# Performance work log

Measured on AMD Instinct MI355X. Metric: run time of the kernel, lower is better.

Reference implementation:

```python
import jax, jax.numpy as jnp
import numpy as np

HIDDEN = 512
EXP = 2048  # hidden * expansion_factor(4)

def _glorot(key, shape):
    fan_in = shape[0]
    return jax.random.normal(key, shape, dtype=jnp.float32) / np.sqrt(fan_in)

def setup_inputs() -> dict:
    key = jax.random.key(0)
    ks = jax.random.split(key, 6)
    B, S = 4, 4096
    return {
        "x": jax.random.normal(ks[0], (B, S, HIDDEN), dtype=jnp.float32),
        "W_in1": _glorot(ks[1], (HIDDEN, EXP)),
        "b_in1": jnp.zeros((EXP,), jnp.float32),
        "W_in2": _glorot(ks[2], (HIDDEN, EXP)),
        "b_in2": jnp.zeros((EXP,), jnp.float32),
        "W_z": _glorot(ks[3], (EXP, EXP)),
        "b_z": jnp.zeros((EXP,), jnp.float32),
        "W_h": _glorot(ks[4], (EXP, EXP)),
        "b_h": jnp.zeros((EXP,), jnp.float32),
        "W_out": _glorot(ks[5], (EXP, HIDDEN)),
        "b_out": jnp.zeros((HIDDEN,), jnp.float32),
    }

def _min_gru(x_in, W_z, b_z, W_h, b_h):
    # minGRU: h_t = (1 - z_t) * h_{t-1} + z_t * h_tilde_t, h_0 = 0
    z = jax.nn.sigmoid(jnp.einsum("bse,ef->bsf", x_in, W_z) + b_z)
    h_tilde = jnp.einsum("bse,ef->bsf", x_in, W_h) + b_h
    a = 1.0 - z          # decay coeff
    b = z * h_tilde      # input term
    def combine(c1, c2):
        a1, b1 = c1
        a2, b2 = c2
        return (a1 * a2, b1 * a2 + b2)
    _, h = jax.lax.associative_scan(combine, (a, b), axis=1)
    return h

def reference(x, W_in1, b_in1, W_in2, b_in2, W_z, b_z, W_h, b_h, W_out, b_out):
    x_in = jax.nn.silu(jnp.einsum("bsd,de->bse", x, W_in1) + b_in1)
    x_skip = jax.nn.silu(jnp.einsum("bsd,de->bse", x, W_in2) + b_in2)
    h = _min_gru(x_in, W_z, b_z, W_h, b_h)
    return jnp.einsum("bse,ed->bsd", x_skip + h, W_out) + b_out
```

## Files before the change

### kernel.cpp

```cpp
#include <hip/hip_runtime.h>
#include <hip/hip_bf16.h>


typedef __bf16 bf16x8 __attribute__((ext_vector_type(8)));
typedef __bf16 bf16x4 __attribute__((ext_vector_type(4)));
typedef float  f32x4  __attribute__((ext_vector_type(4)));

#define DEVINL __device__ __forceinline__

DEVINL void async_ld16(const __bf16* g, __bf16* l) {
    __builtin_amdgcn_global_load_lds(
        (const __attribute__((address_space(1))) void*)g,
        (__attribute__((address_space(3))) void*)l, 16, 0, 0);
}

DEVINL float fsigmoid(float v) { return 1.0f / (1.0f + __expf(-v)); }

template <int MODE>
__global__ __launch_bounds__(256)
void gemm_bt64(const __bf16* __restrict__ A, const __bf16* __restrict__ Bt,
               const float* __restrict__ bias, const float* __restrict__ bias2,
               void* __restrict__ out, void* __restrict__ out2, int N, int K,
               int bps, int seg_stride, int row_off)
{
    struct KL64 { __bf16 A[128 * 64]; __bf16 B[128 * 64]; };
    __shared__ union SMB64 {
        KL64 kl[2];
        __bf16 ct[64 * 136];
    } sm;
    const int tid = threadIdx.x;
    const int bx = blockIdx.x;
    const int seg = bx / bps;
    const int within = bx - seg * bps;
    const int gm0 = row_off + seg * seg_stride + within * 128;
    const int om0 = bx * 128;
    const int n0 = blockIdx.y * 128;

    int rS[4], kS[4];
#pragma unroll
    for (int j = 0; j < 4; ++j) {
        const int s = tid + 256 * j;
        rS[j] = s >> 3;
        kS[j] = (s & 7) ^ (rS[j] & 7);
    }
    const __bf16* Agp[4];
    const __bf16* Bgp[4];
#pragma unroll
    for (int j = 0; j < 4; ++j) {
        Agp[j] = A  + (size_t)(gm0 + rS[j]) * K + kS[j] * 8;
        Bgp[j] = Bt + (size_t)(n0 + rS[j]) * K + kS[j] * 8;
    }

    const int lane = tid & 63;
    const int wave = tid >> 6;
    const int wrow = (wave >> 1) * 64;
    const int wcol = (wave & 1) * 64;
    const int quad = lane >> 4;
    const int r = lane & 15;

    f32x4 acc[4][4] = {};

    const int T = K >> 6;

    auto stage = [&](int t, int b) {
        const int kt = t << 6;
#pragma unroll
        for (int j = 0; j < 4; ++j)
            async_ld16(Agp[j] + kt, sm.kl[b].A + (tid + 256 * j) * 8);
#pragma unroll
        for (int j = 0; j < 4; ++j)
            async_ld16(Bgp[j] + kt, sm.kl[b].B + (tid + 256 * j) * 8);
    };

    stage(0, 0);

    const int swz0 = ((0 * 4 + quad) ^ (r & 7)) * 8;
    const int swz1 = ((1 * 4 + quad) ^ (r & 7)) * 8;

    for (int t = 0; t < T; ++t) {
        const int cur = t & 1;
        if (t + 1 < T) {
            stage(t + 1, cur ^ 1);
            asm volatile("s_waitcnt vmcnt(8)\n\ts_barrier" ::: "memory");
        } else {
            asm volatile("s_waitcnt vmcnt(0)\n\ts_barrier" ::: "memory");
        }

        const __bf16* apb = sm.kl[cur].A + (wrow + r) * 64;
        const __bf16* bpb = sm.kl[cur].B + (wcol + r) * 64;

#pragma unroll
        for (int ks = 0; ks < 2; ++ks) {
            const int swz = ks ? swz1 : swz0;
            bf16x8 af[4], bf_[4];
#pragma unroll
            for (int m = 0; m < 4; ++m)
                af[m] = *(const bf16x8*)(apb + m * 1024 + swz);
#pragma unroll
            for (int n = 0; n < 4; ++n)
                bf_[n] = *(const bf16x8*)(bpb + n * 1024 + swz);

            __builtin_amdgcn_s_setprio(1);
#pragma unroll
            for (int m = 0; m < 4; ++m)
#pragma unroll
                for (int n = 0; n < 4; ++n)
                    acc[m][n] = __builtin_amdgcn_mfma_f32_16x16x32_bf16(
                        af[m], bf_[n], acc[m][n], 0, 0, 0);
            __builtin_amdgcn_s_setprio(0);
        }

        asm volatile("s_waitcnt lgkmcnt(0)\n\ts_barrier" ::: "memory");
    }

    {
        const bool lo = n0 < 2048;
        __bf16* dst = lo ? (__bf16*)out : (__bf16*)out2;
        const int cb = lo ? n0 : n0 - 2048;
        const size_t stride = 2048;
        float bvj[4];
#pragma unroll
        for (int j = 0; j < 4; ++j) {
            const int gc = n0 + wcol + j * 16 + r;
            bvj[j] = lo ? bias[gc] : bias2[gc - 2048];
        }
#pragma unroll
        for (int p = 0; p < 2; ++p) {
#pragma unroll
            for (int ii = 0; ii < 2; ++ii) {
                const int i = 2 * p + ii;
#pragma unroll
                for (int j = 0; j < 4; ++j)
#pragma unroll
                    for (int k = 0; k < 4; ++k) {
                        const float v = acc[i][j][k] + bvj[j];
                        const __bf16 o = (__bf16)(v * fsigmoid(v));
                        sm.ct[((wave >> 1) * 32 + ii * 16 + quad * 4 + k) * 136 +
                              (wcol + j * 16 + r)] = o;
                    }
            }
            __syncthreads();
#pragma unroll
            for (int q = 0; q < 4; ++q) {
                const int chunk = q * 256 + tid;
                const int trow = chunk >> 4;
                const int tc = (chunk & 15) * 8;
                const bf16x8 vv = *(const bf16x8*)(sm.ct + trow * 136 + tc);
                const int grow = om0 + (trow >> 5) * 64 + p * 32 + (trow & 31);
                *(bf16x8*)(dst + (size_t)grow * stride + cb + tc) = vv;
            }
            __syncthreads();
        }
    }
}

template <int MODE>
__global__ __launch_bounds__(512, 2)
void gemm3k(const __bf16* __restrict__ A, const __bf16* __restrict__ Bt,
            const float* __restrict__ bias, const float* __restrict__ bias2,
            void* __restrict__ out, void* __restrict__ out2, int N, int K,
            int bps, int seg_stride, int row_off)
{
    struct KL { __bf16 A[256 * 64]; __bf16 B[256 * 64]; };
    __shared__ union SM3K {
        KL kl[2];
        __bf16 ct[64 * 264];
    } sm;
    const int tid = threadIdx.x;
    const int bx = blockIdx.x;
    const int seg = bx / bps;
    const int within = bx - seg * bps;
    const int gm0 = row_off + seg * seg_stride + within * 256;
    const int om0 = bx * 256;
    const int n0 = blockIdx.y * 256;

    int rA[4], kA[4];
#pragma unroll
    for (int j = 0; j < 4; ++j) {
        const int s = tid + 512 * j;
        rA[j] = s >> 3;
        kA[j] = (s & 7) ^ (rA[j] & 7);
    }
    const __bf16* Agp[4];
    const __bf16* Bgp[4];
#pragma unroll
    for (int j = 0; j < 4; ++j) {
        Agp[j] = A  + (size_t)(gm0 + rA[j]) * K + kA[j] * 8;
        Bgp[j] = Bt + (size_t)(n0 + rA[j]) * K + kA[j] * 8;
    }

    const int lane = tid & 63;
    const int wave = tid >> 6;
    const int wm = wave >> 2;
    const int wn = wave & 3;
    const int quad = lane >> 4;
    const int r = lane & 15;

    f32x4 acc[8][4] = {};

    const int T = K >> 6;

    auto stage = [&](int t, int b) {
        const int kt = t << 6;
#pragma unroll
        for (int j = 0; j < 4; ++j)
            async_ld16(Agp[j] + kt, sm.kl[b].A + (tid + 512 * j) * 8);
#pragma unroll
        for (int j = 0; j < 4; ++j)
            async_ld16(Bgp[j] + kt, sm.kl[b].B + (tid + 512 * j) * 8);
    };

    stage(0, 0);

    const int swz0 = ((0 * 4 + quad) ^ (r & 7)) * 8;
    const int swz1 = ((1 * 4 + quad) ^ (r & 7)) * 8;

    for (int t = 0; t < T; ++t) {
        const int cur = t & 1;
        if (t + 1 < T) {
            stage(t + 1, cur ^ 1);
            asm volatile("s_waitcnt vmcnt(8)\n\ts_barrier" ::: "memory");
        } else {
            asm volatile("s_waitcnt vmcnt(0)\n\ts_barrier" ::: "memory");
        }

        const __bf16* apb = sm.kl[cur].A + (wm * 128 + r) * 64;
        const __bf16* bpb = sm.kl[cur].B + (wn * 64 + r) * 64;

#pragma unroll
        for (int ks = 0; ks < 2; ++ks) {
            const int swz = ks ? swz1 : swz0;
            bf16x8 af[8], bf_[4];
#pragma unroll
            for (int m = 0; m < 8; ++m)
                af[m] = *(const bf16x8*)(apb + m * 1024 + swz);
#pragma unroll
            for (int n = 0; n < 4; ++n)
                bf_[n] = *(const bf16x8*)(bpb + n * 1024 + swz);

            __builtin_amdgcn_s_setprio(1);
#pragma unroll
            for (int m = 0; m < 8; ++m)
#pragma unroll
                for (int n = 0; n < 4; ++n)
                    acc[m][n] = __builtin_amdgcn_mfma_f32_16x16x32_bf16(
                        af[m], bf_[n], acc[m][n], 0, 0, 0);
            __builtin_amdgcn_s_setprio(0);
        }

        asm volatile("s_waitcnt lgkmcnt(0)\n\ts_barrier" ::: "memory");
    }

    __syncthreads();

    const bool lo = n0 < 2048;
    __bf16* dst = (__bf16*)out;
    const int cb = n0;
    const size_t stride = (size_t)N;
    float bvj[4];
#pragma unroll
    for (int nf = 0; nf < 4; ++nf) {
        const int gc = n0 + wn * 64 + nf * 16 + r;
        bvj[nf] = lo ? bias[gc] : bias2[gc - 2048];
    }

#pragma unroll
    for (int p = 0; p < 4; ++p) {
        if (wm == (p >> 1)) {
            const int mb = (p & 1) * 4;
#pragma unroll
            for (int mm = 0; mm < 4; ++mm)
#pragma unroll
                for (int nf = 0; nf < 4; ++nf)
#pragma unroll
                    for (int k = 0; k < 4; ++k) {
                        const float v = acc[mb + mm][nf][k] + bvj[nf];
                        sm.ct[(mm * 16 + quad * 4 + k) * 264 +
                              (wn * 64 + nf * 16 + r)] = (__bf16)v;
                    }
        }
        __syncthreads();
#pragma unroll
        for (int q = 0; q < 4; ++q) {
            const int chunk = q * 512 + tid;
            const int trow = chunk >> 5;
            const int tc = (chunk & 31) * 8;
            const bf16x8 vv = *(const bf16x8*)(sm.ct + trow * 264 + tc);
            *(bf16x8*)(dst + (size_t)(om0 + p * 64 + trow) * stride + cb + tc) = vv;
        }
        __syncthreads();
    }
}

struct KLoopSM { __bf16 A[2][128 * 32]; __bf16 B[2][128 * 32]; };

template <int MODE>
__global__ __launch_bounds__(256)
void gemm_bt(const __bf16* __restrict__ A, const __bf16* __restrict__ Bt,
             const float* __restrict__ bias, const float* __restrict__ bias2,
             void* __restrict__ out, void* __restrict__ out2, int N, int K,
             int bps, int seg_stride, int row_off)
{
    __shared__ union SM {
        KLoopSM kl;
        __bf16 ct[64 * 136];
        float  ctf[32 * 132];
    } sm;
    const int tid = threadIdx.x;
    const int bx = blockIdx.x;
    const int by = blockIdx.y;
    const int seg = bx / bps;
    const int within = bx - seg * bps;
    const int gm0 = row_off + seg * seg_stride + within * 128;
    const int om0 = bx * 128;
    const int n0 = by * 128;

    const int c0 = tid, c1 = tid + 256;
    const int r0 = c0 >> 2, k0 = (c0 & 3) ^ ((c0 >> 3) & 3);
    const int r1 = c1 >> 2, k1 = (c1 & 3) ^ ((c1 >> 3) & 3);
    const __bf16* Ag0 = A  + (size_t)(gm0 + r0) * K + k0 * 8;
    const __bf16* Ag1 = A  + (size_t)(gm0 + r1) * K + k1 * 8;
    const __bf16* Bg0 = Bt + (size_t)(n0 + r0) * K + k0 * 8;
    const __bf16* Bg1 = Bt + (size_t)(n0 + r1) * K + k1 * 8;

    const int lane = tid & 63;
    const int wave = tid >> 6;
    const int wrow = (wave >> 1) * 64;
    const int wcol = (wave & 1) * 64;
    const int quad = lane >> 4;
    const int r = lane & 15;
    const int swz = (quad ^ ((r >> 1) & 3)) * 8;

    f32x4 acc[4][4] = {};

    const int T = K >> 5;
    async_ld16(Ag0, sm.kl.A[0] + c0 * 8);
    async_ld16(Ag1, sm.kl.A[0] + c1 * 8);
    async_ld16(Bg0, sm.kl.B[0] + c0 * 8);
    async_ld16(Bg1, sm.kl.B[0] + c1 * 8);

    for (int t = 0; t < T; ++t) {
        const int cur = t & 1;
        if (t + 1 < T) {
            const int kt = (t + 1) << 5;
            async_ld16(Ag0 + kt, sm.kl.A[cur ^ 1] + c0 * 8);
            async_ld16(Ag1 + kt, sm.kl.A[cur ^ 1] + c1 * 8);
            async_ld16(Bg0 + kt, sm.kl.B[cur ^ 1] + c0 * 8);
            async_ld16(Bg1 + kt, sm.kl.B[cur ^ 1] + c1 * 8);
            asm volatile("s_waitcnt vmcnt(4)\n\ts_barrier" ::: "memory");
        } else {
            asm volatile("s_waitcnt vmcnt(0)\n\ts_barrier" ::: "memory");
        }

        const __bf16* ap = sm.kl.A[cur] + (wrow + r) * 32 + swz;
        const __bf16* bp = sm.kl.B[cur] + (wcol + r) * 32 + swz;
        bf16x8 af[4], bf_[4];
#pragma unroll
        for (int i = 0; i < 4; ++i) af[i] = *(const bf16x8*)(ap + i * 512);
#pragma unroll
        for (int i = 0; i < 4; ++i) bf_[i] = *(const bf16x8*)(bp + i * 512);
#pragma unroll
        for (int i = 0; i < 4; ++i)
#pragma unroll
            for (int j = 0; j < 4; ++j)
                acc[i][j] = __builtin_amdgcn_mfma_f32_16x16x32_bf16(
                    af[i], bf_[j], acc[i][j], 0, 0, 0);

        asm volatile("s_waitcnt lgkmcnt(0)\n\ts_barrier" ::: "memory");
    }

    if (MODE == 3) {
        float bvj[4];
#pragma unroll
        for (int j = 0; j < 4; ++j)
            bvj[j] = bias[n0 + wcol + j * 16 + r];
#pragma unroll
        for (int p = 0; p < 4; ++p) {
#pragma unroll
            for (int j = 0; j < 4; ++j)
#pragma unroll
                for (int k = 0; k < 4; ++k)
                    sm.ctf[((wave >> 1) * 16 + quad * 4 + k) * 132 +
                           (wcol + j * 16 + r)] = acc[p][j][k] + bvj[j];
            __syncthreads();
#pragma unroll
            for (int q = 0; q < 4; ++q) {
                const int chunk = q * 256 + tid;
                const int trow = chunk >> 5;
                const int tc4 = (chunk & 31) * 4;
                const f32x4 vv = *(const f32x4*)(sm.ctf + trow * 132 + tc4);
                const int grow = om0 + (trow >> 4) * 64 + p * 16 + (trow & 15);
                *(f32x4*)((float*)out + (size_t)grow * N + n0 + tc4) = vv;
            }
            __syncthreads();
        }
    } else {
        const bool lo = n0 < 2048;
        __bf16* dst;
        int cb;
        size_t stride;
        if (MODE == 0) {
            dst = lo ? (__bf16*)out : (__bf16*)out2;
            cb = lo ? n0 : n0 - 2048;
            stride = 2048;
        } else {
            dst = (__bf16*)out;
            cb = n0;
            stride = (size_t)N;
        }
        float bvj[4];
#pragma unroll
        for (int j = 0; j < 4; ++j) {
            const int gc = n0 + wcol + j * 16 + r;
            bvj[j] = lo ? bias[gc] : bias2[gc - 2048];
        }
#pragma unroll
        for (int p = 0; p < 2; ++p) {
#pragma unroll
            for (int ii = 0; ii < 2; ++ii) {
                const int i = 2 * p + ii;
#pragma unroll
                for (int j = 0; j < 4; ++j)
#pragma unroll
                    for (int k = 0; k < 4; ++k) {
                        const float v = acc[i][j][k] + bvj[j];
                        const __bf16 o = (MODE == 0) ? (__bf16)(v * fsigmoid(v))
                                                     : (__bf16)v;
                        sm.ct[((wave >> 1) * 32 + ii * 16 + quad * 4 + k) * 136 +
                              (wcol + j * 16 + r)] = o;
                    }
            }
            __syncthreads();
#pragma unroll
            for (int q = 0; q < 4; ++q) {
                const int chunk = q * 256 + tid;
                const int trow = chunk >> 4;
                const int tc = (chunk & 15) * 8;
                const bf16x8 vv = *(const bf16x8*)(sm.ct + trow * 136 + tc);
                const int grow = om0 + (trow >> 5) * 64 + p * 32 + (trow & 31);
                *(bf16x8*)(dst + (size_t)grow * stride + cb + tc) = vv;
            }
            __syncthreads();
        }
    }
}

#define SSEG 32
#define SCOLS 32
__global__ __launch_bounds__(1024)
void scan_kernel(const __bf16* __restrict__ raw, __bf16* __restrict__ xskip,
                 float* __restrict__ carry, int CS, int S, int t0, int first)
{
    __shared__ float Als[SSEG][SCOLS];
    __shared__ float Bls[SSEG][SCOLS];
    const int lane = threadIdx.x & (SCOLS - 1);
    const int w = threadIdx.x >> 5;
    const int nb8 = gridDim.x >> 3;
    const int lin = (blockIdx.x & 7) * nb8 + (blockIdx.x >> 3);
    const int gpb = 2048 / SCOLS;
    const int batch = lin / gpb;
    const int col = (lin - batch * gpb) * SCOLS + lane;
    const int L = CS / SSEG;
    const int tbeg = w * L;

    const size_t rbase = ((size_t)batch * CS + tbeg) * 4096 + col;

    float av[32], bv[32];
    float A = 1.0f, Bv = 0.0f;
    {
        size_t idx = rbase;
#pragma unroll
        for (int t = 0; t < 32; ++t, idx += 4096) {
            const float z = fsigmoid((float)raw[idx]);
            const float b = z * (float)raw[idx + 2048];
            const float a = 1.0f - z;
            av[t] = a;
            bv[t] = b;
            Bv = a * Bv + b;
            A *= a;
        }
    }
    Als[w][lane] = A;
    Bls[w][lane] = Bv;
    __syncthreads();

    const int ch = batch * 2048 + col;
    float h = first ? 0.0f : carry[ch];
    for (int s = 0; s < w; ++s)
        h = Als[s][lane] * h + Bls[s][lane];
    if (w == SSEG - 1)
        carry[ch] = A * h + Bv;

    {
        size_t gidx = ((size_t)batch * S + t0 + tbeg) * 2048 + col;
#pragma unroll
        for (int t = 0; t < 32; ++t, gidx += 2048) {
            h = av[t] * h + bv[t];
            xskip[gidx] = (__bf16)((float)xskip[gidx] + h);
        }
    }
}

__global__ __launch_bounds__(256)
void conv_f32_bf16(const float* __restrict__ x, __bf16* __restrict__ y, int n4)
{
    const int i = blockIdx.x * 256 + threadIdx.x;
    if (i >= n4) return;
    const float4 v = ((const float4*)x)[i];
    bf16x4 o;
    o[0] = (__bf16)v.x; o[1] = (__bf16)v.y; o[2] = (__bf16)v.z; o[3] = (__bf16)v.w;
    ((bf16x4*)y)[i] = o;
}

__global__ __launch_bounds__(256)
void transpose_bf16(const float* __restrict__ W, __bf16* __restrict__ Wt, int K, int N)
{
    __shared__ float tile[32][33];
    const int tx = threadIdx.x & 31;
    const int ty = threadIdx.x >> 5;
    const int nb = blockIdx.x * 32;
    const int kb = blockIdx.y * 32;
#pragma unroll
    for (int i = 0; i < 32; i += 8)
        tile[ty + i][tx] = W[(size_t)(kb + ty + i) * N + nb + tx];
    __syncthreads();
#pragma unroll
    for (int i = 0; i < 32; i += 8)
        Wt[(size_t)(nb + ty + i) * K + kb + tx] = (__bf16)tile[tx][ty + i];
}

extern "C" void kernel_launch(void* const* d_in, const int* in_sizes, int n_in,
                              void* d_out, int out_size, void* d_ws, size_t ws_size,
                              hipStream_t stream)
{
    const float* x     = (const float*)d_in[0];
    const float* W_in1 = (const float*)d_in[1];
    const float* b_in1 = (const float*)d_in[2];
    const float* W_in2 = (const float*)d_in[3];
    const float* b_in2 = (const float*)d_in[4];
    const float* W_z   = (const float*)d_in[5];
    const float* b_z   = (const float*)d_in[6];
    const float* W_h   = (const float*)d_in[7];
    const float* b_h   = (const float*)d_in[8];
    const float* W_out = (const float*)d_in[9];
    const float* b_out = (const float*)d_in[10];

    const int B = 4, S = 4096, H = 512, E = 2048;
    const int M = B * S;
    const int CS = 1024;
    const int NC = S / CS;
    const int MC = B * CS;

    const size_t MiB = 1024 * 1024;
    const size_t NEEDED = 183 * MiB;
    if (ws_size < NEEDED) return;

    char* ws = (char*)d_ws;
    __bf16* xb    = (__bf16*)(ws + 0);
    __bf16* rawzh = (__bf16*)(ws + 0);
    float*  carry = (float*) (ws + 32 * MiB);
    __bf16* xin   = (__bf16*)(ws + 33 * MiB);
    __bf16* xskip = (__bf16*)(ws + 97 * MiB);
    __bf16* Wt12  = (__bf16*)(ws + 161 * MiB);
    __bf16* Wtzh  = (__bf16*)(ws + 165 * MiB);
    __bf16* Wto   = (__bf16*)(ws + 181 * MiB);

    conv_f32_bf16<<<(M * H / 4 + 255) / 256, 256, 0, stream>>>(x, xb, M * H / 4);
    transpose_bf16<<<dim3(E / 32, H / 32), 256, 0, stream>>>(W_in1, Wt12, H, E);
    transpose_bf16<<<dim3(E / 32, H / 32), 256, 0, stream>>>(W_in2, Wt12 + (size_t)E * H, H, E);
    transpose_bf16<<<dim3(E / 32, E / 32), 256, 0, stream>>>(W_z, Wtzh, E, E);
    transpose_bf16<<<dim3(E / 32, E / 32), 256, 0, stream>>>(W_h, Wtzh + (size_t)E * E, E, E);
    transpose_bf16<<<dim3(H / 32, E / 32), 256, 0, stream>>>(W_out, Wto, E, H);

    gemm_bt64<0><<<dim3(M / 128, 2 * E / 128), 256, 0, stream>>>(
        xb, Wt12, b_in1, b_in2, xin, xskip, 2 * E, H, M / 128, 0, 0);

    for (int c = 0; c < NC; ++c) {
        const int row_off = c * CS;
        gemm3k<4><<<dim3(MC / 256, 2 * E / 256), 512, 0, stream>>>(
            xin, Wtzh, b_z, b_h, rawzh, nullptr, 2 * E, E, CS / 256, S, row_off);
        scan_kernel<<<(B * E) / SCOLS, 1024, 0, stream>>>(
            rawzh, xskip, carry, CS, S, row_off, c == 0);
    }

    gemm_bt<3><<<dim3(M / 128, H / 128), 256, 0, stream>>>(
        xskip, Wto, b_out, nullptr, (float*)d_out, nullptr, H, E, M / 128, 0, 0);
}
```

Baseline: 613.5 us.

## Retile input GEMM, use BK64 kernel for output GEMM, fuse prep kernels

The input projection GEMM now runs as a 512-thread kernel with 128x256 tiles and BK=32 in place of 128x128 tiles with BK=64. The output GEMM moves from a BK=32 loop to the BK=64 double-buffered kernel with swizzled 8-chunk layout. The x conversion and five weight transposes are merged into one prep_kernel launch to cut launch overhead. Together these aim to raise MFMA efficiency and reduce per-launch cost, at the price of different occupancy and LDS pressure.

New measurement: 574.7 us. 6.3% less time.

```diff
diff --git a/kernel.cpp b/kernel.cpp
--- a/kernel.cpp
+++ b/kernel.cpp
@@ -17,16 +17,16 @@
 DEVINL float fsigmoid(float v) { return 1.0f / (1.0f + __expf(-v)); }
 
 template <int MODE>
-__global__ __launch_bounds__(256)
-void gemm_bt64(const __bf16* __restrict__ A, const __bf16* __restrict__ Bt,
-               const float* __restrict__ bias, const float* __restrict__ bias2,
-               void* __restrict__ out, void* __restrict__ out2, int N, int K,
-               int bps, int seg_stride, int row_off)
+__global__ __launch_bounds__(512, 4)
+void gemm4(const __bf16* __restrict__ A, const __bf16* __restrict__ Bt,
+           const float* __restrict__ bias, const float* __restrict__ bias2,
+           void* __restrict__ out, void* __restrict__ out2, int N, int K,
+           int bps, int seg_stride, int row_off)
 {
-    struct KL64 { __bf16 A[128 * 64]; __bf16 B[128 * 64]; };
-    __shared__ union SMB64 {
-        KL64 kl[2];
-        __bf16 ct[64 * 136];
+    struct KL { __bf16 A[128 * 32]; __bf16 B[256 * 32]; };
+    __shared__ union SM4 {
+        KL kl[2];
+        __bf16 ct[64 * 264];
     } sm;
     const int tid = threadIdx.x;
     const int bx = blockIdx.x;
@@ -34,123 +34,112 @@
     const int within = bx - seg * bps;
     const int gm0 = row_off + seg * seg_stride + within * 128;
     const int om0 = bx * 128;
-    const int n0 = blockIdx.y * 128;
-
-    int rS[4], kS[4];
-#pragma unroll
-    for (int j = 0; j < 4; ++j) {
-        const int s = tid + 256 * j;
-        rS[j] = s >> 3;
-        kS[j] = (s & 7) ^ (rS[j] & 7);
-    }
-    const __bf16* Agp[4];
-    const __bf16* Bgp[4];
-#pragma unroll
-    for (int j = 0; j < 4; ++j) {
-        Agp[j] = A  + (size_t)(gm0 + rS[j]) * K + kS[j] * 8;
-        Bgp[j] = Bt + (size_t)(n0 + rS[j]) * K + kS[j] * 8;
-    }
+    const int n0 = blockIdx.y * 256;
+
+    const int rA = tid >> 2,         kA = (tid & 3) ^ ((tid >> 3) & 3);
+    const int c0 = tid, c1 = tid + 512;
+    const int rB0 = c0 >> 2,         kB0 = (c0 & 3) ^ ((c0 >> 3) & 3);
+    const int rB1 = c1 >> 2,         kB1 = (c1 & 3) ^ ((c1 >> 3) & 3);
+    const __bf16* Ag  = A  + (size_t)(gm0 + rA)  * K + kA  * 8;
+    const __bf16* Bg0 = Bt + (size_t)(n0 + rB0) * K + kB0 * 8;
+    const __bf16* Bg1 = Bt + (size_t)(n0 + rB1) * K + kB1 * 8;
 
     const int lane = tid & 63;
     const int wave = tid >> 6;
-    const int wrow = (wave >> 1) * 64;
-    const int wcol = (wave & 1) * 64;
+    const int wm = wave >> 2;
+    const int wn = wave & 3;
     const int quad = lane >> 4;
     const int r = lane & 15;
+    const int swz = (quad ^ ((r >> 1) & 3)) * 8;
 
     f32x4 acc[4][4] = {};
 
-    const int T = K >> 6;
+    const int T = K >> 5;
 
     auto stage = [&](int t, int b) {
-        const int kt = t << 6;
-#pragma unroll
-        for (int j = 0; j < 4; ++j)
-            async_ld16(Agp[j] + kt, sm.kl[b].A + (tid + 256 * j) * 8);
-#pragma unroll
-        for (int j = 0; j < 4; ++j)
-            async_ld16(Bgp[j] + kt, sm.kl[b].B + (tid + 256 * j) * 8);
+        const int kt = t << 5;
+        async_ld16(Ag  + kt, sm.kl[b].A + tid * 8);
+        async_ld16(Bg0 + kt, sm.kl[b].B + c0 * 8);
+        async_ld16(Bg1 + kt, sm.kl[b].B + c1 * 8);
     };
 
     stage(0, 0);
-
-    const int swz0 = ((0 * 4 + quad) ^ (r & 7)) * 8;
-    const int swz1 = ((1 * 4 + quad) ^ (r & 7)) * 8;
 
     for (int t = 0; t < T; ++t) {
         const int cur = t & 1;
         if (t + 1 < T) {
             stage(t + 1, cur ^ 1);
-            asm volatile("s_waitcnt vmcnt(8)\n\ts_barrier" ::: "memory");
+            asm volatile("s_waitcnt vmcnt(3)\n\ts_barrier" ::: "memory");
         } else {
             asm volatile("s_waitcnt vmcnt(0)\n\ts_barrier" ::: "memory");
         }
 
-        const __bf16* apb = sm.kl[cur].A + (wrow + r) * 64;
-        const __bf16* bpb = sm.kl[cur].B + (wcol + r) * 64;
-
-#pragma unroll
-        for (int ks = 0; ks < 2; ++ks) {
-            const int swz = ks ? swz1 : swz0;
-            bf16x8 af[4], bf_[4];
-#pragma unroll
-            for (int m = 0; m < 4; ++m)
-                af[m] = *(const bf16x8*)(apb + m * 1024 + swz);
+        const __bf16* ap = sm.kl[cur].A + (wm * 64 + r) * 32 + swz;
+        const __bf16* bp = sm.kl[cur].B + (wn * 64 + r) * 32 + swz;
+        bf16x8 af[4], bf_[4];
+#pragma unroll
+        for (int m = 0; m < 4; ++m) af[m] = *(const bf16x8*)(ap + m * 512);
+#pragma unroll
+        for (int n = 0; n < 4; ++n) bf_[n] = *(const bf16x8*)(bp + n * 512);
+
+        __builtin_amdgcn_s_setprio(1);
+#pragma unroll
+        for (int m = 0; m < 4; ++m)
 #pragma unroll
             for (int n = 0; n < 4; ++n)
-                bf_[n] = *(const bf16x8*)(bpb + n * 1024 + swz);
-
-            __builtin_amdgcn_s_setprio(1);
-#pragma unroll
-            for (int m = 0; m < 4; ++m)
-#pragma unroll
-                for (int n = 0; n < 4; ++n)
-                    acc[m][n] = __builtin_amdgcn_mfma_f32_16x16x32_bf16(
-                        af[m], bf_[n], acc[m][n], 0, 0, 0);
-            __builtin_amdgcn_s_setprio(0);
-        }
+                acc[m][n] = __builtin_amdgcn_mfma_f32_16x16x32_bf16(
+                    af[m], bf_[n], acc[m][n], 0, 0, 0);
+        __builtin_amdgcn_s_setprio(0);
 
         asm volatile("s_waitcnt lgkmcnt(0)\n\ts_barrier" ::: "memory");
     }
 
-    {
-        const bool lo = n0 < 2048;
-        __bf16* dst = lo ? (__bf16*)out : (__bf16*)out2;
-        const int cb = lo ? n0 : n0 - 2048;
-        const size_t stride = 2048;
-        float bvj[4];
-#pragma unroll
-        for (int j = 0; j < 4; ++j) {
-            const int gc = n0 + wcol + j * 16 + r;
-            bvj[j] = lo ? bias[gc] : bias2[gc - 2048];
-        }
-#pragma unroll
-        for (int p = 0; p < 2; ++p) {
-#pragma unroll
-            for (int ii = 0; ii < 2; ++ii) {
-                const int i = 2 * p + ii;
-#pragma unroll
-                for (int j = 0; j < 4; ++j)
+    const bool lo = n0 < 2048;
+    __bf16* dst;
+    int cb;
+    size_t stride;
+    if (MODE == 0) {
+        dst = lo ? (__bf16*)out : (__bf16*)out2;
+        cb = lo ? n0 : n0 - 2048;
+        stride = 2048;
+    } else {
+        dst = (__bf16*)out;
+        cb = n0;
+        stride = (size_t)N;
+    }
+    float bvj[4];
+#pragma unroll
+    for (int nf = 0; nf < 4; ++nf) {
+        const int gc = n0 + wn * 64 + nf * 16 + r;
+        bvj[nf] = lo ? bias[gc] : bias2[gc - 2048];
+    }
+
+#pragma unroll
+    for (int p = 0; p < 2; ++p) {
+        if (wm == p) {
+#pragma unroll
+            for (int mm = 0; mm < 4; ++mm)
+#pragma unroll
+                for (int nf = 0; nf < 4; ++nf)
 #pragma unroll
                     for (int k = 0; k < 4; ++k) {
-                        const float v = acc[i][j][k] + bvj[j];
-                        const __bf16 o = (__bf16)(v * fsigmoid(v));
-                        sm.ct[((wave >> 1) * 32 + ii * 16 + quad * 4 + k) * 136 +
-                              (wcol + j * 16 + r)] = o;
+                        const float v = acc[mm][nf][k] + bvj[nf];
+                        const __bf16 o = (MODE == 0) ? (__bf16)(v * fsigmoid(v))
+                                                     : (__bf16)v;
+                        sm.ct[(mm * 16 + quad * 4 + k) * 264 +
+                              (wn * 64 + nf * 16 + r)] = o;
                     }
-            }
-            __syncthreads();
-#pragma unroll
-            for (int q = 0; q < 4; ++q) {
-                const int chunk = q * 256 + tid;
-                const int trow = chunk >> 4;
-                const int tc = (chunk & 15) * 8;
-                const bf16x8 vv = *(const bf16x8*)(sm.ct + trow * 136 + tc);
-                const int grow = om0 + (trow >> 5) * 64 + p * 32 + (trow & 31);
-                *(bf16x8*)(dst + (size_t)grow * stride + cb + tc) = vv;
-            }
-            __syncthreads();
-        }
+        }
+        __syncthreads();
+#pragma unroll
+        for (int q = 0; q < 4; ++q) {
+            const int chunk = q * 512 + tid;
+            const int trow = chunk >> 5;
+            const int tc = (chunk & 31) * 8;
+            const bf16x8 vv = *(const bf16x8*)(sm.ct + trow * 264 + tc);
+            *(bf16x8*)(dst + (size_t)(om0 + p * 64 + trow) * stride + cb + tc) = vv;
+        }
+        __syncthreads();
     }
 }
 
@@ -292,36 +281,40 @@
     }
 }
 
-struct KLoopSM { __bf16 A[2][128 * 32]; __bf16 B[2][128 * 32]; };
-
 template <int MODE>
 __global__ __launch_bounds__(256)
-void gemm_bt(const __bf16* __restrict__ A, const __bf16* __restrict__ Bt,
-             const float* __restrict__ bias, const float* __restrict__ bias2,
-             void* __restrict__ out, void* __restrict__ out2, int N, int K,
-             int bps, int seg_stride, int row_off)
+void gemm_bt64(const __bf16* __restrict__ A, const __bf16* __restrict__ Bt,
+               const float* __restrict__ bias, const float* __restrict__ bias2,
+               void* __restrict__ out, void* __restrict__ out2, int N, int K,
+               int bps, int seg_stride, int row_off)
 {
-    __shared__ union SM {
-        KLoopSM kl;
-        __bf16 ct[64 * 136];
+    struct KL64 { __bf16 A[128 * 64]; __bf16 B[128 * 64]; };
+    __shared__ union SMB64 {
+        KL64 kl[2];
         float  ctf[32 * 132];
     } sm;
     const int tid = threadIdx.x;
     const int bx = blockIdx.x;
-    const int by = blockIdx.y;
     const int seg = bx / bps;
     const int within = bx - seg * bps;
     const int gm0 = row_off + seg * seg_stride + within * 128;
     const int om0 = bx * 128;
-    const int n0 = by * 128;
-
-    const int c0 = tid, c1 = tid + 256;
-    const int r0 = c0 >> 2, k0 = (c0 & 3) ^ ((c0 >> 3) & 3);
-    const int r1 = c1 >> 2, k1 = (c1 & 3) ^ ((c1 >> 3) & 3);
-    const __bf16* Ag0 = A  + (size_t)(gm0 + r0) * K + k0 * 8;
-    const __bf16* Ag1 = A  + (size_t)(gm0 + r1) * K + k1 * 8;
-    const __bf16* Bg0 = Bt + (size_t)(n0 + r0) * K + k0 * 8;
-    const __bf16* Bg1 = Bt + (size_t)(n0 + r1) * K + k1 * 8;
+    const int n0 = blockIdx.y * 128;
+
+    int rS[4], kS[4];
+#pragma unroll
+    for (int j = 0; j < 4; ++j) {
+        const int s = tid + 256 * j;
+        rS[j] = s >> 3;
+        kS[j] = (s & 7) ^ (rS[j] & 7);
+    }
+    const __bf16* Agp[4];
+    const __bf16* Bgp[4];
+#pragma unroll
+    for (int j = 0; j < 4; ++j) {
+        Agp[j] = A  + (size_t)(gm0 + rS[j]) * K + kS[j] * 8;
+        Bgp[j] = Bt + (size_t)(n0 + rS[j]) * K + kS[j] * 8;
+    }
 
     const int lane = tid & 63;
     const int wave = tid >> 6;
@@ -329,47 +322,63 @@
     const int wcol = (wave & 1) * 64;
     const int quad = lane >> 4;
     const int r = lane & 15;
-    const int swz = (quad ^ ((r >> 1) & 3)) * 8;
 
     f32x4 acc[4][4] = {};
 
-    const int T = K >> 5;
-    async_ld16(Ag0, sm.kl.A[0] + c0 * 8);
-    async_ld16(Ag1, sm.kl.A[0] + c1 * 8);
-    async_ld16(Bg0, sm.kl.B[0] + c0 * 8);
-    async_ld16(Bg1, sm.kl.B[0] + c1 * 8);
+    const int T = K >> 6;
+
+    auto stage = [&](int t, int b) {
+        const int kt = t << 6;
+#pragma unroll
+        for (int j = 0; j < 4; ++j)
+            async_ld16(Agp[j] + kt, sm.kl[b].A + (tid + 256 * j) * 8);
+#pragma unroll
+        for (int j = 0; j < 4; ++j)
+            async_ld16(Bgp[j] + kt, sm.kl[b].B + (tid + 256 * j) * 8);
+    };
+
+    stage(0, 0);
+
+    const int swz0 = ((0 * 4 + quad) ^ (r & 7)) * 8;
+    const int swz1 = ((1 * 4 + quad) ^ (r & 7)) * 8;
 
     for (int t = 0; t < T; ++t) {
         const int cur = t & 1;
         if (t + 1 < T) {
-            const int kt = (t + 1) << 5;
-            async_ld16(Ag0 + kt, sm.kl.A[cur ^ 1] + c0 * 8);
-            async_ld16(Ag1 + kt, sm.kl.A[cur ^ 1] + c1 * 8);
-            async_ld16(Bg0 + kt, sm.kl.B[cur ^ 1] + c0 * 8);
-            async_ld16(Bg1 + kt, sm.kl.B[cur ^ 1] + c1 * 8);
-            asm volatile("s_waitcnt vmcnt(4)\n\ts_barrier" ::: "memory");
+            stage(t + 1, cur ^ 1);
+            asm volatile("s_waitcnt vmcnt(8)\n\ts_barrier" ::: "memory");
         } else {
             asm volatile("s_waitcnt vmcnt(0)\n\ts_barrier" ::: "memory");
         }
 
-        const __bf16* ap = sm.kl.A[cur] + (wrow + r) * 32 + swz;
-        const __bf16* bp = sm.kl.B[cur] + (wcol + r) * 32 + swz;
-        bf16x8 af[4], bf_[4];
-#pragma unroll
-        for (int i = 0; i < 4; ++i) af[i] = *(const bf16x8*)(ap + i * 512);
-#pragma unroll
-        for (int i = 0; i < 4; ++i) bf_[i] = *(const bf16x8*)(bp + i * 512);
-#pragma unroll
-        for (int i = 0; i < 4; ++i)
-#pragma unroll
-            for (int j = 0; j < 4; ++j)
-                acc[i][j] = __builtin_amdgcn_mfma_f32_16x16x32_bf16(
-                    af[i], bf_[j], acc[i][j], 0, 0, 0);
+        const __bf16* apb = sm.kl[cur].A + (wrow + r) * 64;
+        const __bf16* bpb = sm.kl[cur].B + (wcol + r) * 64;
+
+#pragma unroll
+        for (int ks = 0; ks < 2; ++ks) {
+            const int swz = ks ? swz1 : swz0;
+            bf16x8 af[4], bf_[4];
+#pragma unroll
+            for (int m = 0; m < 4; ++m)
+                af[m] = *(const bf16x8*)(apb + m * 1024 + swz);
+#pragma unroll
+            for (int n = 0; n < 4; ++n)
+                bf_[n] = *(const bf16x8*)(bpb + n * 1024 + swz);
+
+            __builtin_amdgcn_s_setprio(1);
+#pragma unroll
+            for (int m = 0; m < 4; ++m)
+#pragma unroll
+                for (int n = 0; n < 4; ++n)
+                    acc[m][n] = __builtin_amdgcn_mfma_f32_16x16x32_bf16(
+                        af[m], bf_[n], acc[m][n], 0, 0, 0);
+            __builtin_amdgcn_s_setprio(0);
+        }
 
         asm volatile("s_waitcnt lgkmcnt(0)\n\ts_barrier" ::: "memory");
     }
 
-    if (MODE == 3) {
+    {
         float bvj[4];
 #pragma unroll
         for (int j = 0; j < 4; ++j)
@@ -391,54 +400,6 @@
                 const f32x4 vv = *(const f32x4*)(sm.ctf + trow * 132 + tc4);
                 const int grow = om0 + (trow >> 4) * 64 + p * 16 + (trow & 15);
                 *(f32x4*)((float*)out + (size_t)grow * N + n0 + tc4) = vv;
-            }
-            __syncthreads();
-        }
-    } else {
-        const bool lo = n0 < 2048;
-        __bf16* dst;
-        int cb;
-        size_t stride;
-        if (MODE == 0) {
-            dst = lo ? (__bf16*)out : (__bf16*)out2;
-            cb = lo ? n0 : n0 - 2048;
-            stride = 2048;
-        } else {
-            dst = (__bf16*)out;
-            cb = n0;
-            stride = (size_t)N;
-        }
-        float bvj[4];
-#pragma unroll
-        for (int j = 0; j < 4; ++j) {
-            const int gc = n0 + wcol + j * 16 + r;
-            bvj[j] = lo ? bias[gc] : bias2[gc - 2048];
-        }
-#pragma unroll
-        for (int p = 0; p < 2; ++p) {
-#pragma unroll
-            for (int ii = 0; ii < 2; ++ii) {
-                const int i = 2 * p + ii;
-#pragma unroll
-                for (int j = 0; j < 4; ++j)
-#pragma unroll
-                    for (int k = 0; k < 4; ++k) {
-                        const float v = acc[i][j][k] + bvj[j];
-                        const __bf16 o = (MODE == 0) ? (__bf16)(v * fsigmoid(v))
-                                                     : (__bf16)v;
-                        sm.ct[((wave >> 1) * 32 + ii * 16 + quad * 4 + k) * 136 +
-                              (wcol + j * 16 + r)] = o;
-                    }
-            }
-            __syncthreads();
-#pragma unroll
-            for (int q = 0; q < 4; ++q) {
-                const int chunk = q * 256 + tid;
-                const int trow = chunk >> 4;
-                const int tc = (chunk & 15) * 8;
-                const bf16x8 vv = *(const bf16x8*)(sm.ct + trow * 136 + tc);
-                const int grow = om0 + (trow >> 5) * 64 + p * 32 + (trow & 31);
-                *(bf16x8*)(dst + (size_t)grow * stride + cb + tc) = vv;
             }
             __syncthreads();
         }
@@ -502,31 +463,56 @@
 }
 
 __global__ __launch_bounds__(256)
-void conv_f32_bf16(const float* __restrict__ x, __bf16* __restrict__ y, int n4)
-{
-    const int i = blockIdx.x * 256 + threadIdx.x;
-    if (i >= n4) return;
-    const float4 v = ((const float4*)x)[i];
-    bf16x4 o;
-    o[0] = (__bf16)v.x; o[1] = (__bf16)v.y; o[2] = (__bf16)v.z; o[3] = (__bf16)v.w;
-    ((bf16x4*)y)[i] = o;
-}
-
-__global__ __launch_bounds__(256)
-void transpose_bf16(const float* __restrict__ W, __bf16* __restrict__ Wt, int K, int N)
+void prep_kernel(const float* __restrict__ x, __bf16* __restrict__ xb,
+                 const float* __restrict__ W_in1, const float* __restrict__ W_in2,
+                 __bf16* __restrict__ Wt12,
+                 const float* __restrict__ W_z, const float* __restrict__ W_h,
+                 __bf16* __restrict__ Wtzh,
+                 const float* __restrict__ W_out, __bf16* __restrict__ Wto)
 {
     __shared__ float tile[32][33];
+    int bid = blockIdx.x;
+    if (bid < 8192) {
+        const int i = bid * 256 + threadIdx.x;
+        const float4 v = ((const float4*)x)[i];
+        bf16x4 o;
+        o[0] = (__bf16)v.x; o[1] = (__bf16)v.y;
+        o[2] = (__bf16)v.z; o[3] = (__bf16)v.w;
+        ((bf16x4*)xb)[i] = o;
+        return;
+    }
+    bid -= 8192;
+    const float* W;
+    __bf16* dst;
+    int K, N, nb, kb;
+    if (bid < 2048) {
+        const int z = bid >> 10, rem = bid & 1023;
+        W = z ? W_in2 : W_in1;
+        dst = Wt12 + (size_t)z * 512 * 2048;
+        K = 512; N = 2048;
+        nb = (rem & 63) * 32; kb = (rem >> 6) * 32;
+    } else if (bid < 2048 + 8192) {
+        const int b2 = bid - 2048;
+        const int z = b2 >> 12, rem = b2 & 4095;
+        W = z ? W_h : W_z;
+        dst = Wtzh + (size_t)z * 2048 * 2048;
+        K = 2048; N = 2048;
+        nb = (rem & 63) * 32; kb = (rem >> 6) * 32;
+    } else {
+        const int b3 = bid - (2048 + 8192);
+        W = W_out; dst = Wto;
+        K = 2048; N = 512;
+        nb = (b3 & 15) * 32; kb = (b3 >> 4) * 32;
+    }
     const int tx = threadIdx.x & 31;
     const int ty = threadIdx.x >> 5;
-    const int nb = blockIdx.x * 32;
-    const int kb = blockIdx.y * 32;
 #pragma unroll
     for (int i = 0; i < 32; i += 8)
         tile[ty + i][tx] = W[(size_t)(kb + ty + i) * N + nb + tx];
     __syncthreads();
 #pragma unroll
     for (int i = 0; i < 32; i += 8)
-        Wt[(size_t)(nb + ty + i) * K + kb + tx] = (__bf16)tile[tx][ty + i];
+        dst[(size_t)(nb + ty + i) * K + kb + tx] = (__bf16)tile[tx][ty + i];
 }
 
 extern "C" void kernel_launch(void* const* d_in, const int* in_sizes, int n_in,
@@ -565,14 +551,10 @@
     __bf16* Wtzh  = (__bf16*)(ws + 165 * MiB);
     __bf16* Wto   = (__bf16*)(ws + 181 * MiB);
 
-    conv_f32_bf16<<<(M * H / 4 + 255) / 256, 256, 0, stream>>>(x, xb, M * H / 4);
-    transpose_bf16<<<dim3(E / 32, H / 32), 256, 0, stream>>>(W_in1, Wt12, H, E);
-    transpose_bf16<<<dim3(E / 32, H / 32), 256, 0, stream>>>(W_in2, Wt12 + (size_t)E * H, H, E);
-    transpose_bf16<<<dim3(E / 32, E / 32), 256, 0, stream>>>(W_z, Wtzh, E, E);
-    transpose_bf16<<<dim3(E / 32, E / 32), 256, 0, stream>>>(W_h, Wtzh + (size_t)E * E, E, E);
-    transpose_bf16<<<dim3(H / 32, E / 32), 256, 0, stream>>>(W_out, Wto, E, H);
-
-    gemm_bt64<0><<<dim3(M / 128, 2 * E / 128), 256, 0, stream>>>(
+    prep_kernel<<<8192 + 2048 + 8192 + 1024, 256, 0, stream>>>(
+        x, xb, W_in1, W_in2, Wt12, W_z, W_h, Wtzh, W_out, Wto);
+
+    gemm4<0><<<dim3(M / 128, 2 * E / 256), 512, 0, stream>>>(
         xb, Wt12, b_in1, b_in2, xin, xskip, 2 * E, H, M / 128, 0, 0);
 
     for (int c = 0; c < NC; ++c) {
@@ -583,6 +565,6 @@
             rawzh, xskip, carry, CS, S, row_off, c == 0);
     }
 
-    gemm_bt<3><<<dim3(M / 128, H / 128), 256, 0, stream>>>(
+    gemm_bt64<3><<<dim3(M / 128, H / 128), 256, 0, stream>>>(
         xskip, Wto, b_out, nullptr, (float*)d_out, nullptr, H, E, M / 128, 0, 0);
 }
```
